# Performance work log

Measured on AMD Instinct MI355X. Metric: run time of the kernel, lower is better.

## Reference

```python
import jax, jax.numpy as jnp
import numpy as np

B, H, W, C = 2, 256, 256, 96
NH, WS, SS = 3, 8, 4
HD = C // NH
N = WS * WS              # tokens per window
NWIMG = (H // WS) * (W // WS)  # windows per image
MLP = 4 * C
EPS = 1e-5

def _np_attn_mask():
    img = np.zeros((H, W))
    sl = (slice(0, -WS), slice(-WS, -SS), slice(-SS, None))
    cnt = 0
    for a in sl:
        for b in sl:
            img[a, b] = cnt
            cnt += 1
    m = img.reshape(H // WS, WS, W // WS, WS).transpose(0, 2, 1, 3).reshape(-1, N)
    am = m[:, None, :] - m[:, :, None]
    return np.where(am != 0, -100.0, 0.0).astype(np.float32)

def _np_rel_index():
    coords = np.stack(np.meshgrid(np.arange(WS), np.arange(WS), indexing='ij'))
    cf = coords.reshape(2, -1)
    rel = (cf[:, :, None] - cf[:, None, :]).transpose(1, 2, 0).copy()
    rel[..., 0] += WS - 1
    rel[..., 1] += WS - 1
    rel[..., 0] *= 2 * WS - 1
    return rel.sum(-1)

def _np_coords_table():
    r = np.arange(-(WS - 1), WS, dtype=np.float32)
    t = np.stack(np.meshgrid(r, r, indexing='ij'), axis=-1) / (WS - 1) * 8.0
    t = np.sign(t) * np.log2(np.abs(t) + 1.0) / np.log2(8.0)
    return t.reshape(-1, 2)

ATTN_MASK = jnp.asarray(_np_attn_mask())          # [NWIMG, N, N]
REL_INDEX = jnp.asarray(_np_rel_index().reshape(-1))
COORDS_TABLE = jnp.asarray(_np_coords_table())    # [(2WS-1)^2, 2]

def setup_inputs():
    key = jax.random.key(0)
    ks = jax.random.split(key, 16)
    s = 0.02
    return {
        'hidden_states': jax.random.normal(ks[0], (B, H * W, C), jnp.float32),
        'time': jax.random.uniform(ks[1], (B,), jnp.float32),
        'q_w': jax.random.normal(ks[2], (C, C), jnp.float32) * s,
        'q_b': jnp.zeros((C,), jnp.float32),
        'k_w': jax.random.normal(ks[3], (C, C), jnp.float32) * s,
        'v_w': jax.random.normal(ks[4], (C, C), jnp.float32) * s,
        'v_b': jnp.zeros((C,), jnp.float32),
        'proj_w': jax.random.normal(ks[5], (C, C), jnp.float32) * s,
        'proj_b': jnp.zeros((C,), jnp.float32),
        'logit_scale': jnp.full((NH, 1, 1), jnp.log(10.0), jnp.float32),
        'cpb_w1': jax.random.normal(ks[6], (2, 512), jnp.float32) * s,
        'cpb_b1': jnp.zeros((512,), jnp.float32),
        'cpb_w2': jax.random.normal(ks[7], (512, NH), jnp.float32) * s,
        'lnb_ww': jax.random.normal(ks[8], (1, C), jnp.float32) * s,
        'lnb_wb': jnp.ones((C,), jnp.float32),
        'lnb_bw': jax.random.normal(ks[9], (1, C), jnp.float32) * s,
        'lnb_bb': jnp.zeros((C,), jnp.float32),
        'lna_ww': jax.random.normal(ks[10], (1, C), jnp.float32) * s,
        'lna_wb': jnp.ones((C,), jnp.float32),
        'lna_bw': jax.random.normal(ks[11], (1, C), jnp.float32) * s,
        'lna_bb': jnp.zeros((C,), jnp.float32),
        'fc1_w': jax.random.normal(ks[12], (C, MLP), jnp.float32) * s,
        'fc1_b': jnp.zeros((MLP,), jnp.float32),
        'fc2_w': jax.random.normal(ks[13], (MLP, C), jnp.float32) * s,
        'fc2_b': jnp.zeros((C,), jnp.float32),
    }

def _cln(x, time, ww, wb, bw, bb):
    # ConditionalLayerNorm: stats over channels, affine params from time via Linear(1, C)
    mean = x.mean(-1, keepdims=True)
    var = (x * x).mean(-1, keepdims=True) - mean * mean
    xn = (x - mean) / jnp.sqrt(var + EPS)
    t = time.reshape(-1, 1)
    w = (t @ ww + wb)[:, None, :]
    b = (t @ bw + bb)[:, None, :]
    return w * xn + b

def reference(hidden_states, time, q_w, q_b, k_w, v_w, v_b, proj_w, proj_b, logit_scale, cpb_w1, cpb_b1, cpb_w2, lnb_ww, lnb_wb, lnb_bw, lnb_bb, lna_ww, lna_wb, lna_bw, lna_bb, fc1_w, fc1_b, fc2_w, fc2_b):
    shortcut = hidden_states
    x = hidden_states.reshape(B, H, W, C)
    x = jnp.roll(x, (-SS, -SS), axis=(1, 2))  # cyclic shift
    # window partition -> [nW, N, C]
    xw = x.reshape(B, H // WS, WS, W // WS, WS, C).transpose(0, 1, 3, 2, 4, 5).reshape(-1, N, C)
    nW = B * NWIMG
    q = (xw @ q_w + q_b).reshape(nW, N, NH, HD).transpose(0, 2, 1, 3)
    k = (xw @ k_w).reshape(nW, N, NH, HD).transpose(0, 2, 1, 3)  # key has no bias in Swinv2
    v = (xw @ v_w + v_b).reshape(nW, N, NH, HD).transpose(0, 2, 1, 3)
    # cosine attention with clamped learnable log temperature
    qn = q / jnp.maximum(jnp.linalg.norm(q, axis=-1, keepdims=True), 1e-12)
    kn = k / jnp.maximum(jnp.linalg.norm(k, axis=-1, keepdims=True), 1e-12)
    scale = jnp.exp(jnp.minimum(logit_scale, jnp.log(100.0)))  # [NH,1,1]
    attn = jnp.einsum('whnd,whmd->whnm', qn, kn) * scale[None]
    # continuous relative position bias: MLP(2->512->NH) over log-spaced coords
    bias_table = jax.nn.relu(COORDS_TABLE @ cpb_w1 + cpb_b1) @ cpb_w2
    bias = bias_table[REL_INDEX].reshape(N, N, NH).transpose(2, 0, 1)
    attn = attn + 16.0 * jax.nn.sigmoid(bias)[None]
    # shifted-window mask
    attn = attn.reshape(B, NWIMG, NH, N, N) + ATTN_MASK[None, :, None]
    attn = jax.nn.softmax(attn.reshape(nW, NH, N, N), axis=-1)
    ctx = jnp.einsum('whnm,whmd->whnd', attn, v).transpose(0, 2, 1, 3).reshape(nW, N, C)
    ctx = ctx @ proj_w + proj_b
    # window reverse + un-shift
    xr = ctx.reshape(B, H // WS, W // WS, WS, WS, C).transpose(0, 1, 3, 2, 4, 5).reshape(B, H, W, C)
    xr = jnp.roll(xr, (SS, SS), axis=(1, 2))
    attn_out = xr.reshape(B, H * W, C)
    # post-norm residual (Swin v2 style) with conditional LN
    hs = shortcut + _cln(attn_out, time, lnb_ww, lnb_wb, lnb_bw, lnb_bb)
    inter = jax.nn.gelu(hs @ fc1_w + fc1_b, approximate=False)
    mlp_out = inter @ fc2_w + fc2_b
    return hs + _cln(mlp_out, time, lna_ww, lna_wb, lna_bw, lna_bb)
```

## Files before the change

kernel.cpp:

```cpp
#include <hip/hip_runtime.h>
#include <hip/hip_bf16.h>

typedef __bf16 bf16_t;
typedef bf16_t bf16x8 __attribute__((ext_vector_type(8)));
typedef bf16_t bf16x4 __attribute__((ext_vector_type(4)));
typedef float  f32x4  __attribute__((ext_vector_type(4)));

#define LDC 104
#define LDT 72

#define WS_WQ    0
#define WS_WK    19968
#define WS_WV    39936
#define WS_WP    59904
#define WS_FC1   79872
#define WS_FC2   159744
#define WS_BIAS  239616

__device__ __forceinline__ f32x4 mfma16(bf16x8 a, bf16x8 b, f32x4 c) {
    return __builtin_amdgcn_mfma_f32_16x16x32_bf16(a, b, c, 0, 0, 0);
}

__device__ __forceinline__ float cpbf(int v) {
    float x = (float)v * (8.0f / 7.0f);
    float l = log2f(fabsf(x) + 1.0f) * (1.0f / 3.0f);
    return x < 0.f ? -l : l;
}

__device__ __forceinline__ int regcnt(int t, int hw, int ww) {
    int r = t >> 3, c = t & 7;
    int rr = (hw == 31) ? (r < 4 ? 1 : 2) : 0;
    int cc = (ww == 31) ? (c < 4 ? 1 : 2) : 0;
    return rr * 3 + cc;
}

__global__ __launch_bounds__(512) void k0_prep(
    const float* __restrict__ qw, const float* __restrict__ kw,
    const float* __restrict__ vw, const float* __restrict__ pw,
    const float* __restrict__ fc1w, const float* __restrict__ fc2w,
    const float* __restrict__ cw1, const float* __restrict__ cb1,
    const float* __restrict__ cw2, char* __restrict__ ws)
{
    int tid = threadIdx.x;
    if (blockIdx.x == 0) {
        __shared__ float part[450 * 3];
        __shared__ float table[225 * 3];
        if (tid < 450) {
            int pos = tid >> 1, half = tid & 1;
            int ia = pos / 15, ib = pos % 15;
            float c0 = cpbf(ia - 7), c1 = cpbf(ib - 7);
            float a0 = 0.f, a1 = 0.f, a2 = 0.f;
            int j0 = half * 256;
            for (int j = j0; j < j0 + 256; ++j) {
                float h = fmaf(c0, cw1[j], fmaf(c1, cw1[512 + j], cb1[j]));
                h = fmaxf(h, 0.f);
                a0 = fmaf(h, cw2[j * 3 + 0], a0);
                a1 = fmaf(h, cw2[j * 3 + 1], a1);
                a2 = fmaf(h, cw2[j * 3 + 2], a2);
            }
            part[tid * 3 + 0] = a0; part[tid * 3 + 1] = a1; part[tid * 3 + 2] = a2;
        }
        __syncthreads();
        if (tid < 225) {
            table[tid * 3 + 0] = part[(2 * tid) * 3 + 0] + part[(2 * tid + 1) * 3 + 0];
            table[tid * 3 + 1] = part[(2 * tid) * 3 + 1] + part[(2 * tid + 1) * 3 + 1];
            table[tid * 3 + 2] = part[(2 * tid) * 3 + 2] + part[(2 * tid + 1) * 3 + 2];
        }
        __syncthreads();
        float* bias = (float*)(ws + WS_BIAS);
        for (int e = tid; e < 3 * 64 * 64; e += 512) {
            int h = e >> 12, nm = e & 4095, n = nm >> 6, m = nm & 63;
            int dr = (n >> 3) - (m >> 3) + 7, dc = (n & 7) - (m & 7) + 7;
            float t = table[(dr * 15 + dc) * 3 + h];
            bias[e] = 16.f / (1.f + __expf(-t));
        }
    } else {
        int idx = (blockIdx.x - 1) * 512 + tid;
        if (idx < 36864) {
            int which = idx / 9216, r = idx % 9216;
            int o = r / 96, i = r % 96;
            const float* src = which == 0 ? qw : which == 1 ? kw : which == 2 ? vw : pw;
            ((bf16_t*)(ws + WS_WQ + which * 19968))[o * LDC + i] = (bf16_t)src[i * 96 + o];
        } else if (idx < 73728) {
            int r = idx - 36864;
            int o = r / 96, i = r % 96;
            ((bf16_t*)(ws + WS_FC1))[o * LDC + i] = (bf16_t)fc1w[i * 384 + o];
        } else if (idx < 110592) {
            int r = idx - 73728;
            int ks = r / 9216, rr = r % 9216, o = rr / 96, j = rr % 96;
            ((bf16_t*)(ws + WS_FC2))[(ks * 96 + o) * LDC + j] = (bf16_t)fc2w[(ks * 96 + j) * 96 + o];
        }
    }
}

__global__ __launch_bounds__(256, 3) void kA_attn(
    const float* __restrict__ hidden, const float* __restrict__ tv,
    const float* __restrict__ qb, const float* __restrict__ vb,
    const float* __restrict__ pb, const float* __restrict__ lsc,
    const float* __restrict__ lnww, const float* __restrict__ lnwb,
    const float* __restrict__ lnbw, const float* __restrict__ lnbb,
    const char* __restrict__ ws, float* __restrict__ hs)
{
    __shared__ __align__(16) char sm[53760];
    bf16_t* xwb  = (bf16_t*)(sm + 0);
    bf16_t* qn   = (bf16_t*)(sm + 13312);
    bf16_t* kn   = (bf16_t*)(sm + 26624);
    bf16_t* vT   = (bf16_t*)(sm + 39936);
    bf16_t* P    = (bf16_t*)(sm + 0);
    bf16_t* ctxb = (bf16_t*)(sm + 39936);

    const int tid = threadIdx.x;
    const int wv = tid >> 6, lane = tid & 63, lg = lane >> 4, lr = lane & 15;
    const int wid = blockIdx.x;
    const int bat = wid >> 10, wim = wid & 1023, hw = wim >> 5, wwi = wim & 31;

    #pragma unroll
    for (int i = 0; i < 6; ++i) {
        int idx = tid + 256 * i;
        int t = idx / 24, grp = idx - t * 24;
        int gr = ((hw << 3) + (t >> 3) + 4) & 255;
        int gc = ((wwi << 3) + (t & 7) + 4) & 255;
        const float4 v = *(const float4*)(hidden + (((size_t)bat << 16) + (gr << 8) + gc) * 96 + grp * 4);
        bf16x4 p; p[0] = (bf16_t)v.x; p[1] = (bf16_t)v.y; p[2] = (bf16_t)v.z; p[3] = (bf16_t)v.w;
        *(bf16x4*)(xwb + t * LDC + grp * 4) = p;
    }
    __syncthreads();

    {
        bf16x8 af[3];
        #pragma unroll
        for (int ks = 0; ks < 3; ++ks) af[ks] = *(const bf16x8*)(xwb + (16 * wv + lr) * LDC + 32 * ks + 8 * lg);
        const bf16_t* Wq = (const bf16_t*)(ws + WS_WQ);
        const bf16_t* Wk = (const bf16_t*)(ws + WS_WK);
        const bf16_t* Wv = (const bf16_t*)(ws + WS_WV);

        #pragma unroll
        for (int h = 0; h < 3; ++h) {
            f32x4 a0 = {0.f,0.f,0.f,0.f}, a1 = {0.f,0.f,0.f,0.f};
            #pragma unroll
            for (int ks = 0; ks < 3; ++ks) {
                a0 = mfma16(af[ks], *(const bf16x8*)(Wq + (32 * h + lr) * LDC + 32 * ks + 8 * lg), a0);
                a1 = mfma16(af[ks], *(const bf16x8*)(Wq + (32 * h + 16 + lr) * LDC + 32 * ks + 8 * lg), a1);
            }
            float b0 = qb[32 * h + lr], b1 = qb[32 * h + 16 + lr];
            #pragma unroll
            for (int j = 0; j < 4; ++j) { a0[j] += b0; a1[j] += b1; }
            #pragma unroll
            for (int j = 0; j < 4; ++j) {
                float s = a0[j] * a0[j] + a1[j] * a1[j];
                s += __shfl_xor(s, 1); s += __shfl_xor(s, 2); s += __shfl_xor(s, 4); s += __shfl_xor(s, 8);
                float inv = 1.f / fmaxf(sqrtf(s), 1e-12f);
                int row = 16 * wv + 4 * lg + j;
                qn[row * LDC + 32 * h + lr]      = (bf16_t)(a0[j] * inv);
                qn[row * LDC + 32 * h + 16 + lr] = (bf16_t)(a1[j] * inv);
            }
        }
        #pragma unroll
        for (int h = 0; h < 3; ++h) {
            f32x4 a0 = {0.f,0.f,0.f,0.f}, a1 = {0.f,0.f,0.f,0.f};
            #pragma unroll
            for (int ks = 0; ks < 3; ++ks) {
                a0 = mfma16(af[ks], *(const bf16x8*)(Wk + (32 * h + lr) * LDC + 32 * ks + 8 * lg), a0);
                a1 = mfma16(af[ks], *(const bf16x8*)(Wk + (32 * h + 16 + lr) * LDC + 32 * ks + 8 * lg), a1);
            }
            #pragma unroll
            for (int j = 0; j < 4; ++j) {
                float s = a0[j] * a0[j] + a1[j] * a1[j];
                s += __shfl_xor(s, 1); s += __shfl_xor(s, 2); s += __shfl_xor(s, 4); s += __shfl_xor(s, 8);
                float inv = 1.f / fmaxf(sqrtf(s), 1e-12f);
                int row = 16 * wv + 4 * lg + j;
                kn[row * LDC + 32 * h + lr]      = (bf16_t)(a0[j] * inv);
                kn[row * LDC + 32 * h + 16 + lr] = (bf16_t)(a1[j] * inv);
            }
        }
        #pragma unroll
        for (int nt = 0; nt < 6; ++nt) {
            f32x4 a = {0.f,0.f,0.f,0.f};
            #pragma unroll
            for (int ks = 0; ks < 3; ++ks)
                a = mfma16(af[ks], *(const bf16x8*)(Wv + (16 * nt + lr) * LDC + 32 * ks + 8 * lg), a);
            float bv_ = vb[16 * nt + lr];
            bf16x4 pk;
            #pragma unroll
            for (int j = 0; j < 4; ++j) pk[j] = (bf16_t)(a[j] + bv_);
            *(bf16x4*)(vT + (16 * nt + lr) * LDT + 16 * wv + 4 * lg) = pk;
        }
    }
    __syncthreads();

    {
        bf16x8 aq[3], bk[3][4];
        #pragma unroll
        for (int h = 0; h < 3; ++h) {
            aq[h] = *(const bf16x8*)(qn + (16 * wv + lr) * LDC + 32 * h + 8 * lg);
            #pragma unroll
            for (int f = 0; f < 4; ++f)
                bk[h][f] = *(const bf16x8*)(kn + (16 * f + lr) * LDC + 32 * h + 8 * lg);
        }
        __syncthreads();

        float ls[3];
        #pragma unroll
        for (int h = 0; h < 3; ++h) ls[h] = __expf(fminf(lsc[h], 4.6051702f));
        f32x4 s[3][4];
        #pragma unroll
        for (int h = 0; h < 3; ++h)
            #pragma unroll
            for (int f = 0; f < 4; ++f) {
                f32x4 z = {0.f,0.f,0.f,0.f};
                s[h][f] = mfma16(aq[h], bk[h][f], z);
            }
        const float* biasT = (const float*)(ws + WS_BIAS);
        int cntm[4], cnti[4];
        #pragma unroll
        for (int f = 0; f < 4; ++f) cntm[f] = regcnt(16 * f + lr, hw, wwi);
        #pragma unroll
        for (int j = 0; j < 4; ++j) cnti[j] = regcnt(16 * wv + 4 * lg + j, hw, wwi);
        #pragma unroll
        for (int h = 0; h < 3; ++h) {
            #pragma unroll
            for (int f = 0; f < 4; ++f)
                #pragma unroll
                for (int j = 0; j < 4; ++j) {
                    float b = biasT[(h << 12) + (16 * wv + 4 * lg + j) * 64 + 16 * f + lr];
                    float mk = (cnti[j] != cntm[f]) ? -100.f : 0.f;
                    s[h][f][j] = fmaf(s[h][f][j], ls[h], b + mk);
                }
            #pragma unroll
            for (int j = 0; j < 4; ++j) {
                float mx = fmaxf(fmaxf(s[h][0][j], s[h][1][j]), fmaxf(s[h][2][j], s[h][3][j]));
                mx = fmaxf(mx, __shfl_xor(mx, 1)); mx = fmaxf(mx, __shfl_xor(mx, 2));
                mx = fmaxf(mx, __shfl_xor(mx, 4)); mx = fmaxf(mx, __shfl_xor(mx, 8));
                float sum = 0.f;
                #pragma unroll
                for (int f = 0; f < 4; ++f) { float e = __expf(s[h][f][j] - mx); s[h][f][j] = e; sum += e; }
                sum += __shfl_xor(sum, 1); sum += __shfl_xor(sum, 2); sum += __shfl_xor(sum, 4); sum += __shfl_xor(sum, 8);
                float inv = 1.f / sum;
                int row = 16 * wv + 4 * lg + j;
                #pragma unroll
                for (int f = 0; f < 4; ++f)
                    P[h * 64 * LDT + row * LDT + 16 * f + lr] = (bf16_t)(s[h][f][j] * inv);
            }
        }
    }
    __syncthreads();

    {
        bf16x8 ap[3][2], bv2[3][2][2];
        #pragma unroll
        for (int h = 0; h < 3; ++h)
            #pragma unroll
            for (int ks = 0; ks < 2; ++ks) {
                ap[h][ks] = *(const bf16x8*)(P + h * 64 * LDT + (16 * wv + lr) * LDT + 32 * ks + 8 * lg);
                #pragma unroll
                for (int dt = 0; dt < 2; ++dt)
                    bv2[h][dt][ks] = *(const bf16x8*)(vT + (32 * h + 16 * dt + lr) * LDT + 32 * ks + 8 * lg);
            }
        f32x4 ctx[6];
        #pragma unroll
        for (int t = 0; t < 6; ++t) { f32x4 z = {0.f,0.f,0.f,0.f}; ctx[t] = z; }
        #pragma unroll
        for (int h = 0; h < 3; ++h)
            #pragma unroll
            for (int ks = 0; ks < 2; ++ks)
                #pragma unroll
                for (int dt = 0; dt < 2; ++dt)
                    ctx[2 * h + dt] = mfma16(ap[h][ks], bv2[h][dt][ks], ctx[2 * h + dt]);
        __syncthreads();
        #pragma unroll
        for (int t = 0; t < 6; ++t)
            #pragma unroll
            for (int j = 0; j < 4; ++j)
                ctxb[(16 * wv + 4 * lg + j) * LDC + 16 * t + lr] = (bf16_t)ctx[t][j];
    }
    __syncthreads();

    {
        const bf16_t* Wp = (const bf16_t*)(ws + WS_WP);
        bf16x8 af[3];
        #pragma unroll
        for (int ks = 0; ks < 3; ++ks) af[ks] = *(const bf16x8*)(ctxb + (16 * wv + lr) * LDC + 32 * ks + 8 * lg);
        f32x4 acc[6];
        #pragma unroll
        for (int nt = 0; nt < 6; ++nt) {
            f32x4 a = {0.f,0.f,0.f,0.f};
            #pragma unroll
            for (int ks = 0; ks < 3; ++ks)
                a = mfma16(af[ks], *(const bf16x8*)(Wp + (16 * nt + lr) * LDC + 32 * ks + 8 * lg), a);
            float bp = pb[16 * nt + lr];
            #pragma unroll
            for (int j = 0; j < 4; ++j) a[j] += bp;
            acc[nt] = a;
        }
        float tb = tv[bat];
        #pragma unroll
        for (int j = 0; j < 4; ++j) {
            float smn = 0.f, sq = 0.f;
            #pragma unroll
            for (int t = 0; t < 6; ++t) { float v = acc[t][j]; smn += v; sq = fmaf(v, v, sq); }
            smn += __shfl_xor(smn, 1); smn += __shfl_xor(smn, 2); smn += __shfl_xor(smn, 4); smn += __shfl_xor(smn, 8);
            sq  += __shfl_xor(sq, 1);  sq  += __shfl_xor(sq, 2);  sq  += __shfl_xor(sq, 4);  sq  += __shfl_xor(sq, 8);
            float mean = smn * (1.f / 96.f);
            float var  = sq * (1.f / 96.f) - mean * mean;
            float rstd = rsqrtf(var + 1e-5f);
            int trow = 16 * wv + 4 * lg + j;
            int gr = ((hw << 3) + (trow >> 3) + 4) & 255;
            int gc = ((wwi << 3) + (trow & 7) + 4) & 255;
            size_t gbase = (((size_t)bat << 16) + (gr << 8) + gc) * 96;
            #pragma unroll
            for (int t = 0; t < 6; ++t) {
                int col = 16 * t + lr;
                float w = fmaf(tb, lnww[col], lnwb[col]);
                float b = fmaf(tb, lnbw[col], lnbb[col]);
                float xn = (acc[t][j] - mean) * rstd;
                hs[gbase + col] = hidden[gbase + col] + fmaf(w, xn, b);
            }
        }
    }
}

__global__ __launch_bounds__(256, 4) void kB_mlp(
    const float* __restrict__ tv, const float* __restrict__ fc1b,
    const float* __restrict__ fc2b,
    const float* __restrict__ lnww, const float* __restrict__ lnwb,
    const float* __restrict__ lnbw, const float* __restrict__ lnbb,
    const char* __restrict__ ws, float* __restrict__ io)
{
    __shared__ __align__(16) bf16_t gbuf[64 * LDC];

    const int tid = threadIdx.x;
    const int wv = tid >> 6, lane = tid & 63, lg = lane >> 4, lr = lane & 15;
    const size_t t0 = (size_t)blockIdx.x * 64;

    bf16x8 hf[3];
    #pragma unroll
    for (int ks = 0; ks < 3; ++ks) {
        const float* p = io + (t0 + 16 * wv + lr) * 96 + 32 * ks + 8 * lg;
        float4 u0 = *(const float4*)p;
        float4 u1 = *(const float4*)(p + 4);
        bf16x8 f;
        f[0] = (bf16_t)u0.x; f[1] = (bf16_t)u0.y; f[2] = (bf16_t)u0.z; f[3] = (bf16_t)u0.w;
        f[4] = (bf16_t)u1.x; f[5] = (bf16_t)u1.y; f[6] = (bf16_t)u1.z; f[7] = (bf16_t)u1.w;
        hf[ks] = f;
    }

    f32x4 mlp[6];
    #pragma unroll
    for (int t = 0; t < 6; ++t) { f32x4 z = {0.f,0.f,0.f,0.f}; mlp[t] = z; }
    const bf16_t* w1 = (const bf16_t*)(ws + WS_FC1);
    const bf16_t* w2 = (const bf16_t*)(ws + WS_FC2);

    for (int ch = 0; ch < 4; ++ch) {
        if (ch) __syncthreads();
        #pragma unroll
        for (int nt = 0; nt < 6; ++nt) {
            f32x4 a = {0.f,0.f,0.f,0.f};
            #pragma unroll
            for (int ks = 0; ks < 3; ++ks)
                a = mfma16(hf[ks], *(const bf16x8*)(w1 + (ch * 96 + 16 * nt + lr) * LDC + 32 * ks + 8 * lg), a);
            float bb = fc1b[ch * 96 + 16 * nt + lr];
            #pragma unroll
            for (int j = 0; j < 4; ++j) {
                float x = a[j] + bb;
                float u = 0.7978845608f * fmaf(0.044715f * x, x * x, x);
                float t = __expf(2.f * u);
                float g = x - x * __builtin_amdgcn_rcpf(t + 1.f);
                gbuf[(16 * wv + 4 * lg + j) * LDC + 16 * nt + lr] = (bf16_t)g;
            }
        }
        __syncthreads();
        #pragma unroll
        for (int ks = 0; ks < 3; ++ks) {
            bf16x8 gf = *(const bf16x8*)(gbuf + (16 * wv + lr) * LDC + 32 * ks + 8 * lg);
            #pragma unroll
            for (int nt = 0; nt < 6; ++nt)
                mlp[nt] = mfma16(gf, *(const bf16x8*)(w2 + (ch * 96 + 16 * nt + lr) * LDC + 32 * ks + 8 * lg), mlp[nt]);
        }
    }

    float tb = tv[t0 >> 16];
    #pragma unroll
    for (int nt = 0; nt < 6; ++nt) {
        float bb = fc2b[16 * nt + lr];
        #pragma unroll
        for (int j = 0; j < 4; ++j) mlp[nt][j] += bb;
    }
    #pragma unroll
    for (int j = 0; j < 4; ++j) {
        float smn = 0.f, sq = 0.f;
        #pragma unroll
        for (int t = 0; t < 6; ++t) { float v = mlp[t][j]; smn += v; sq = fmaf(v, v, sq); }
        smn += __shfl_xor(smn, 1); smn += __shfl_xor(smn, 2); smn += __shfl_xor(smn, 4); smn += __shfl_xor(smn, 8);
        sq  += __shfl_xor(sq, 1);  sq  += __shfl_xor(sq, 2);  sq  += __shfl_xor(sq, 4);  sq  += __shfl_xor(sq, 8);
        float mean = smn * (1.f / 96.f);
        float var  = sq * (1.f / 96.f) - mean * mean;
        float rstd = rsqrtf(var + 1e-5f);
        size_t row = t0 + 16 * wv + 4 * lg + j;
        #pragma unroll
        for (int t = 0; t < 6; ++t) {
            int col = 16 * t + lr;
            float w = fmaf(tb, lnww[col], lnwb[col]);
            float b = fmaf(tb, lnbw[col], lnbb[col]);
            float xn = (mlp[t][j] - mean) * rstd;
            io[row * 96 + col] = io[row * 96 + col] + fmaf(w, xn, b);
        }
    }
}

extern "C" void kernel_launch(void* const* d_in, const int* in_sizes, int n_in,
                              void* d_out, int out_size, void* d_ws, size_t ws_size,
                              hipStream_t stream)
{
    const float* hidden = (const float*)d_in[0];
    const float* tv     = (const float*)d_in[1];
    const float* q_w    = (const float*)d_in[2];
    const float* q_b    = (const float*)d_in[3];
    const float* k_w    = (const float*)d_in[4];
    const float* v_w    = (const float*)d_in[5];
    const float* v_b    = (const float*)d_in[6];
    const float* p_w    = (const float*)d_in[7];
    const float* p_b    = (const float*)d_in[8];
    const float* lsc    = (const float*)d_in[9];
    const float* cw1    = (const float*)d_in[10];
    const float* cb1    = (const float*)d_in[11];
    const float* cw2    = (const float*)d_in[12];
    const float* lnb_ww = (const float*)d_in[13];
    const float* lnb_wb = (const float*)d_in[14];
    const float* lnb_bw = (const float*)d_in[15];
    const float* lnb_bb = (const float*)d_in[16];
    const float* lna_ww = (const float*)d_in[17];
    const float* lna_wb = (const float*)d_in[18];
    const float* lna_bw = (const float*)d_in[19];
    const float* lna_bb = (const float*)d_in[20];
    const float* fc1_b  = (const float*)d_in[22];
    const float* fc2_b  = (const float*)d_in[24];
    const float* fc1_w  = (const float*)d_in[21];
    const float* fc2_w  = (const float*)d_in[23];
    char* ws = (char*)d_ws;
    float* out = (float*)d_out;

    k0_prep<<<dim3(217), dim3(512), 0, stream>>>(q_w, k_w, v_w, p_w, fc1_w, fc2_w, cw1, cb1, cw2, ws);
    kA_attn<<<dim3(2048), dim3(256), 0, stream>>>(hidden, tv, q_b, v_b, p_b, lsc,
                                                  lnb_ww, lnb_wb, lnb_bw, lnb_bb, ws, out);
    kB_mlp<<<dim3(2048), dim3(256), 0, stream>>>(tv, fc1_b, fc2_b,
                                                 lna_ww, lna_wb, lna_bw, lna_bb, ws, out);
}
```

Measured before the change: 326.6 us.

## Shrink attention LDS, load A fragments directly, unchunk MLP hidden buffer

The attention kernel now builds the X fragments straight from global memory instead of staging the window in shared memory. It reorders the LDS layout and reduces P's padding, which shrinks shared memory so four blocks fit per CU, and it interleaves the score and PV loads per head to lower register pressure. The MLP kernel now computes the full 384-wide GELU activation into a larger LDS buffer before one fc2 pass. This removes the per-chunk barriers but lowers occupancy to three blocks per CU. The weight prep now reads float4s in row order and uses fewer blocks, with fc2 laid out in a single LDG-stride matrix.

New measurement: 332.1 us. No clear change (+1.7%).

```diff
diff --git a/kernel.cpp b/kernel.cpp
--- a/kernel.cpp
+++ b/kernel.cpp
@@ -8,6 +8,8 @@
 
 #define LDC 104
 #define LDT 72
+#define LDP 70
+#define LDG 392
 
 #define WS_WQ    0
 #define WS_WK    19968
@@ -15,7 +17,7 @@
 #define WS_WP    59904
 #define WS_FC1   79872
 #define WS_FC2   159744
-#define WS_BIAS  239616
+#define WS_BIAS  235008
 
 __device__ __forceinline__ f32x4 mfma16(bf16x8 a, bf16x8 b, f32x4 c) {
     return __builtin_amdgcn_mfma_f32_16x16x32_bf16(a, b, c, 0, 0, 0);
@@ -75,25 +77,40 @@
             bias[e] = 16.f / (1.f + __expf(-t));
         }
     } else {
-        int idx = (blockIdx.x - 1) * 512 + tid;
-        if (idx < 36864) {
-            int which = idx / 9216, r = idx % 9216;
-            int o = r / 96, i = r % 96;
+        int rid = (blockIdx.x - 1) * 512 + tid;
+        if (rid < 9216) {
+            int which = rid / 2304, r = rid % 2304;
+            int i = r / 24, o4 = r % 24;
             const float* src = which == 0 ? qw : which == 1 ? kw : which == 2 ? vw : pw;
-            ((bf16_t*)(ws + WS_WQ + which * 19968))[o * LDC + i] = (bf16_t)src[i * 96 + o];
-        } else if (idx < 73728) {
-            int r = idx - 36864;
-            int o = r / 96, i = r % 96;
-            ((bf16_t*)(ws + WS_FC1))[o * LDC + i] = (bf16_t)fc1w[i * 384 + o];
-        } else if (idx < 110592) {
-            int r = idx - 73728;
-            int ks = r / 9216, rr = r % 9216, o = rr / 96, j = rr % 96;
-            ((bf16_t*)(ws + WS_FC2))[(ks * 96 + o) * LDC + j] = (bf16_t)fc2w[(ks * 96 + j) * 96 + o];
-        }
-    }
-}
-
-__global__ __launch_bounds__(256, 3) void kA_attn(
+            float4 u = *(const float4*)(src + i * 96 + 4 * o4);
+            bf16_t* dst = (bf16_t*)(ws + WS_WQ + which * 19968);
+            dst[(4 * o4 + 0) * LDC + i] = (bf16_t)u.x;
+            dst[(4 * o4 + 1) * LDC + i] = (bf16_t)u.y;
+            dst[(4 * o4 + 2) * LDC + i] = (bf16_t)u.z;
+            dst[(4 * o4 + 3) * LDC + i] = (bf16_t)u.w;
+        } else if (rid < 18432) {
+            int r = rid - 9216;
+            int i = r / 96, m4 = r % 96;
+            float4 u = *(const float4*)(fc1w + i * 384 + 4 * m4);
+            bf16_t* dst = (bf16_t*)(ws + WS_FC1);
+            dst[(4 * m4 + 0) * LDC + i] = (bf16_t)u.x;
+            dst[(4 * m4 + 1) * LDC + i] = (bf16_t)u.y;
+            dst[(4 * m4 + 2) * LDC + i] = (bf16_t)u.z;
+            dst[(4 * m4 + 3) * LDC + i] = (bf16_t)u.w;
+        } else {
+            int r = rid - 18432;
+            int g = r / 24, o4 = r % 24;
+            float4 u = *(const float4*)(fc2w + g * 96 + 4 * o4);
+            bf16_t* dst = (bf16_t*)(ws + WS_FC2);
+            dst[(4 * o4 + 0) * LDG + g] = (bf16_t)u.x;
+            dst[(4 * o4 + 1) * LDG + g] = (bf16_t)u.y;
+            dst[(4 * o4 + 2) * LDG + g] = (bf16_t)u.z;
+            dst[(4 * o4 + 3) * LDG + g] = (bf16_t)u.w;
+        }
+    }
+}
+
+__global__ __launch_bounds__(256, 4) void kA_attn(
     const float* __restrict__ hidden, const float* __restrict__ tv,
     const float* __restrict__ qb, const float* __restrict__ vb,
     const float* __restrict__ pb, const float* __restrict__ lsc,
@@ -101,35 +118,35 @@
     const float* __restrict__ lnbw, const float* __restrict__ lnbb,
     const char* __restrict__ ws, float* __restrict__ hs)
 {
-    __shared__ __align__(16) char sm[53760];
-    bf16_t* xwb  = (bf16_t*)(sm + 0);
-    bf16_t* qn   = (bf16_t*)(sm + 13312);
-    bf16_t* kn   = (bf16_t*)(sm + 26624);
-    bf16_t* vT   = (bf16_t*)(sm + 39936);
-    bf16_t* P    = (bf16_t*)(sm + 0);
-    bf16_t* ctxb = (bf16_t*)(sm + 39936);
+    __shared__ __align__(16) char sm[40704];
+    bf16_t* vT   = (bf16_t*)(sm + 0);
+    bf16_t* qn   = (bf16_t*)(sm + 13824);
+    bf16_t* kn   = (bf16_t*)(sm + 27136);
+    bf16_t* P    = (bf16_t*)(sm + 13824);
+    bf16_t* ctxb = (bf16_t*)(sm + 0);
 
     const int tid = threadIdx.x;
     const int wv = tid >> 6, lane = tid & 63, lg = lane >> 4, lr = lane & 15;
     const int wid = blockIdx.x;
     const int bat = wid >> 10, wim = wid & 1023, hw = wim >> 5, wwi = wim & 31;
 
-    #pragma unroll
-    for (int i = 0; i < 6; ++i) {
-        int idx = tid + 256 * i;
-        int t = idx / 24, grp = idx - t * 24;
-        int gr = ((hw << 3) + (t >> 3) + 4) & 255;
-        int gc = ((wwi << 3) + (t & 7) + 4) & 255;
-        const float4 v = *(const float4*)(hidden + (((size_t)bat << 16) + (gr << 8) + gc) * 96 + grp * 4);
-        bf16x4 p; p[0] = (bf16_t)v.x; p[1] = (bf16_t)v.y; p[2] = (bf16_t)v.z; p[3] = (bf16_t)v.w;
-        *(bf16x4*)(xwb + t * LDC + grp * 4) = p;
-    }
-    __syncthreads();
-
     {
         bf16x8 af[3];
-        #pragma unroll
-        for (int ks = 0; ks < 3; ++ks) af[ks] = *(const bf16x8*)(xwb + (16 * wv + lr) * LDC + 32 * ks + 8 * lg);
+        {
+            int tok = 16 * wv + lr;
+            int gr = ((hw << 3) + (tok >> 3) + 4) & 255;
+            int gc = ((wwi << 3) + (tok & 7) + 4) & 255;
+            const float* xb = hidden + (((size_t)bat << 16) + (gr << 8) + gc) * 96;
+            #pragma unroll
+            for (int ks = 0; ks < 3; ++ks) {
+                float4 u0 = *(const float4*)(xb + 32 * ks + 8 * lg);
+                float4 u1 = *(const float4*)(xb + 32 * ks + 8 * lg + 4);
+                bf16x8 f;
+                f[0] = (bf16_t)u0.x; f[1] = (bf16_t)u0.y; f[2] = (bf16_t)u0.z; f[3] = (bf16_t)u0.w;
+                f[4] = (bf16_t)u1.x; f[5] = (bf16_t)u1.y; f[6] = (bf16_t)u1.z; f[7] = (bf16_t)u1.w;
+                af[ks] = f;
+            }
+        }
         const bf16_t* Wq = (const bf16_t*)(ws + WS_WQ);
         const bf16_t* Wk = (const bf16_t*)(ws + WS_WK);
         const bf16_t* Wv = (const bf16_t*)(ws + WS_WV);
@@ -189,27 +206,25 @@
     __syncthreads();
 
     {
-        bf16x8 aq[3], bk[3][4];
+        f32x4 s[3][4];
         #pragma unroll
         for (int h = 0; h < 3; ++h) {
-            aq[h] = *(const bf16x8*)(qn + (16 * wv + lr) * LDC + 32 * h + 8 * lg);
+            bf16x8 aq = *(const bf16x8*)(qn + (16 * wv + lr) * LDC + 32 * h + 8 * lg);
+            bf16x8 bk[4];
             #pragma unroll
             for (int f = 0; f < 4; ++f)
-                bk[h][f] = *(const bf16x8*)(kn + (16 * f + lr) * LDC + 32 * h + 8 * lg);
-        }
-        __syncthreads();
-
-        float ls[3];
-        #pragma unroll
-        for (int h = 0; h < 3; ++h) ls[h] = __expf(fminf(lsc[h], 4.6051702f));
-        f32x4 s[3][4];
-        #pragma unroll
-        for (int h = 0; h < 3; ++h)
+                bk[f] = *(const bf16x8*)(kn + (16 * f + lr) * LDC + 32 * h + 8 * lg);
             #pragma unroll
             for (int f = 0; f < 4; ++f) {
                 f32x4 z = {0.f,0.f,0.f,0.f};
-                s[h][f] = mfma16(aq[h], bk[h][f], z);
-            }
+                s[h][f] = mfma16(aq, bk[f], z);
+            }
+        }
+        __syncthreads();
+
+        float ls[3];
+        #pragma unroll
+        for (int h = 0; h < 3; ++h) ls[h] = __expf(fminf(lsc[h], 4.6051702f));
         const float* biasT = (const float*)(ws + WS_BIAS);
         int cntm[4], cnti[4];
         #pragma unroll
@@ -239,33 +254,32 @@
                 int row = 16 * wv + 4 * lg + j;
                 #pragma unroll
                 for (int f = 0; f < 4; ++f)
-                    P[h * 64 * LDT + row * LDT + 16 * f + lr] = (bf16_t)(s[h][f][j] * inv);
+                    P[h * 64 * LDP + row * LDP + 16 * f + lr] = (bf16_t)(s[h][f][j] * inv);
             }
         }
     }
     __syncthreads();
 
     {
-        bf16x8 ap[3][2], bv2[3][2][2];
-        #pragma unroll
-        for (int h = 0; h < 3; ++h)
+        f32x4 ctx[6];
+        #pragma unroll
+        for (int t = 0; t < 6; ++t) { f32x4 z = {0.f,0.f,0.f,0.f}; ctx[t] = z; }
+        #pragma unroll
+        for (int h = 0; h < 3; ++h) {
+            bf16x8 ap[2], bv2[2][2];
             #pragma unroll
             for (int ks = 0; ks < 2; ++ks) {
-                ap[h][ks] = *(const bf16x8*)(P + h * 64 * LDT + (16 * wv + lr) * LDT + 32 * ks + 8 * lg);
+                ap[ks] = *(const bf16x8*)(P + h * 64 * LDP + (16 * wv + lr) * LDP + 32 * ks + 8 * lg);
                 #pragma unroll
                 for (int dt = 0; dt < 2; ++dt)
-                    bv2[h][dt][ks] = *(const bf16x8*)(vT + (32 * h + 16 * dt + lr) * LDT + 32 * ks + 8 * lg);
-            }
-        f32x4 ctx[6];
-        #pragma unroll
-        for (int t = 0; t < 6; ++t) { f32x4 z = {0.f,0.f,0.f,0.f}; ctx[t] = z; }
-        #pragma unroll
-        for (int h = 0; h < 3; ++h)
+                    bv2[dt][ks] = *(const bf16x8*)(vT + (32 * h + 16 * dt + lr) * LDT + 32 * ks + 8 * lg);
+            }
             #pragma unroll
             for (int ks = 0; ks < 2; ++ks)
                 #pragma unroll
                 for (int dt = 0; dt < 2; ++dt)
-                    ctx[2 * h + dt] = mfma16(ap[h][ks], bv2[h][dt][ks], ctx[2 * h + dt]);
+                    ctx[2 * h + dt] = mfma16(ap[ks], bv2[dt][ks], ctx[2 * h + dt]);
+        }
         __syncthreads();
         #pragma unroll
         for (int t = 0; t < 6; ++t)
@@ -319,14 +333,14 @@
     }
 }
 
-__global__ __launch_bounds__(256, 4) void kB_mlp(
+__global__ __launch_bounds__(256, 3) void kB_mlp(
     const float* __restrict__ tv, const float* __restrict__ fc1b,
     const float* __restrict__ fc2b,
     const float* __restrict__ lnww, const float* __restrict__ lnwb,
     const float* __restrict__ lnbw, const float* __restrict__ lnbb,
     const char* __restrict__ ws, float* __restrict__ io)
 {
-    __shared__ __align__(16) bf16_t gbuf[64 * LDC];
+    __shared__ __align__(16) bf16_t gbuf[64 * LDG];
 
     const int tid = threadIdx.x;
     const int wv = tid >> 6, lane = tid & 63, lg = lane >> 4, lr = lane & 15;
@@ -344,38 +358,36 @@
         hf[ks] = f;
     }
 
+    const bf16_t* w1 = (const bf16_t*)(ws + WS_FC1);
+    const bf16_t* w2 = (const bf16_t*)(ws + WS_FC2);
+
+    #pragma unroll 6
+    for (int nt = 0; nt < 24; ++nt) {
+        f32x4 a = {0.f,0.f,0.f,0.f};
+        #pragma unroll
+        for (int ks = 0; ks < 3; ++ks)
+            a = mfma16(hf[ks], *(const bf16x8*)(w1 + (16 * nt + lr) * LDC + 32 * ks + 8 * lg), a);
+        float bb = fc1b[16 * nt + lr];
+        #pragma unroll
+        for (int j = 0; j < 4; ++j) {
+            float x = a[j] + bb;
+            float u = 0.7978845608f * fmaf(0.044715f * x, x * x, x);
+            float t = __expf(2.f * u);
+            float g = x - x * __builtin_amdgcn_rcpf(t + 1.f);
+            gbuf[(16 * wv + 4 * lg + j) * LDG + 16 * nt + lr] = (bf16_t)g;
+        }
+    }
+    __syncthreads();
+
     f32x4 mlp[6];
     #pragma unroll
     for (int t = 0; t < 6; ++t) { f32x4 z = {0.f,0.f,0.f,0.f}; mlp[t] = z; }
-    const bf16_t* w1 = (const bf16_t*)(ws + WS_FC1);
-    const bf16_t* w2 = (const bf16_t*)(ws + WS_FC2);
-
-    for (int ch = 0; ch < 4; ++ch) {
-        if (ch) __syncthreads();
-        #pragma unroll
-        for (int nt = 0; nt < 6; ++nt) {
-            f32x4 a = {0.f,0.f,0.f,0.f};
-            #pragma unroll
-            for (int ks = 0; ks < 3; ++ks)
-                a = mfma16(hf[ks], *(const bf16x8*)(w1 + (ch * 96 + 16 * nt + lr) * LDC + 32 * ks + 8 * lg), a);
-            float bb = fc1b[ch * 96 + 16 * nt + lr];
-            #pragma unroll
-            for (int j = 0; j < 4; ++j) {
-                float x = a[j] + bb;
-                float u = 0.7978845608f * fmaf(0.044715f * x, x * x, x);
-                float t = __expf(2.f * u);
-                float g = x - x * __builtin_amdgcn_rcpf(t + 1.f);
-                gbuf[(16 * wv + 4 * lg + j) * LDC + 16 * nt + lr] = (bf16_t)g;
-            }
-        }
-        __syncthreads();
-        #pragma unroll
-        for (int ks = 0; ks < 3; ++ks) {
-            bf16x8 gf = *(const bf16x8*)(gbuf + (16 * wv + lr) * LDC + 32 * ks + 8 * lg);
-            #pragma unroll
-            for (int nt = 0; nt < 6; ++nt)
-                mlp[nt] = mfma16(gf, *(const bf16x8*)(w2 + (ch * 96 + 16 * nt + lr) * LDC + 32 * ks + 8 * lg), mlp[nt]);
-        }
+    #pragma unroll
+    for (int kk = 0; kk < 12; ++kk) {
+        bf16x8 gf = *(const bf16x8*)(gbuf + (16 * wv + lr) * LDG + 32 * kk + 8 * lg);
+        #pragma unroll
+        for (int nt = 0; nt < 6; ++nt)
+            mlp[nt] = mfma16(gf, *(const bf16x8*)(w2 + (16 * nt + lr) * LDG + 32 * kk + 8 * lg), mlp[nt]);
     }
 
     float tb = tv[t0 >> 16];
@@ -432,14 +444,14 @@
     const float* lna_wb = (const float*)d_in[18];
     const float* lna_bw = (const float*)d_in[19];
     const float* lna_bb = (const float*)d_in[20];
+    const float* fc1_w  = (const float*)d_in[21];
     const float* fc1_b  = (const float*)d_in[22];
+    const float* fc2_w  = (const float*)d_in[23];
     const float* fc2_b  = (const float*)d_in[24];
-    const float* fc1_w  = (const float*)d_in[21];
-    const float* fc2_w  = (const float*)d_in[23];
     char* ws = (char*)d_ws;
     float* out = (float*)d_out;
 
-    k0_prep<<<dim3(217), dim3(512), 0, stream>>>(q_w, k_w, v_w, p_w, fc1_w, fc2_w, cw1, cb1, cw2, ws);
+    k0_prep<<<dim3(55), dim3(512), 0, stream>>>(q_w, k_w, v_w, p_w, fc1_w, fc2_w, cw1, cb1, cw2, ws);
     kA_attn<<<dim3(2048), dim3(256), 0, stream>>>(hidden, tv, q_b, v_b, p_b, lsc,
                                                   lnb_ww, lnb_wb, lnb_bw, lnb_bb, ws, out);
     kB_mlp<<<dim3(2048), dim3(256), 0, stream>>>(tv, fc1_b, fc2_b,
```
